# Kernel tuning notes

Measured on AMD Instinct MI355X. Metric: run time of the kernel, lower is better.

## Reference

```python
import jax, jax.numpy as jnp
import numpy as np

# HGIN_classifier: two relational-GIN layers with ReLU between.
# FastRGIN layer math (relational GIN, eps=0, single-linear MLP):
#   agg_r[i] = sum_{(j->i) with edge_type r} x[j]          (per-relation neighbor sum)
#   out[i]   = (1+eps) * x[i] @ W_self + sum_r agg_r[i] @ W_r + b

N = 100000      # nodes
E = 1600000     # edges (avg degree 16)
R = 2           # relations (follower / following)
DIN, DH, DOUT = 128, 256, 2
EPS = 0.0


def setup_inputs() -> dict:
    key = jax.random.key(0)
    ks = jax.random.split(key, 8)
    x = jax.random.normal(ks[0], (N, DIN), dtype=jnp.float32)
    edge_index = jax.random.randint(ks[1], (2, E), 0, N, dtype=jnp.int64)
    edge_type = jax.random.randint(ks[2], (E,), 0, R, dtype=jnp.int64)
    s1 = 1.0 / np.sqrt(DIN).astype(np.float32)
    s2 = 1.0 / np.sqrt(DH).astype(np.float32)
    w1_self = jax.random.normal(ks[3], (DIN, DH), jnp.float32) * s1
    w1_rel = jax.random.normal(ks[4], (R, DIN, DH), jnp.float32) * s1
    b1 = jnp.zeros((DH,), jnp.float32)
    w2_self = jax.random.normal(ks[5], (DH, DOUT), jnp.float32) * s2
    w2_rel = jax.random.normal(ks[6], (R, DH, DOUT), jnp.float32) * s2
    b2 = jnp.zeros((DOUT,), jnp.float32)
    return {"x": x, "edge_index": edge_index, "edge_type": edge_type,
            "w1_self": w1_self, "w1_rel": w1_rel, "b1": b1,
            "w2_self": w2_self, "w2_rel": w2_rel, "b2": b2}


def _rgin_layer(x, src, dst, etype, w_self, w_rel, b):
    n = x.shape[0]
    r = w_rel.shape[0]
    # fused (node, relation) segment id so one segment_sum handles all relations
    seg = dst * r + etype                                   # [E]
    agg = jax.ops.segment_sum(x[src], seg, num_segments=n * r)  # [N*R, d_in]
    agg = agg.reshape(n, r, -1)                              # [N, R, d_in]
    return (1.0 + EPS) * (x @ w_self) + jnp.einsum('nri,rio->no', agg, w_rel) + b


def reference(x, edge_index, edge_type, w1_self, w1_rel, b1, w2_self, w2_rel, b2):
    src, dst = edge_index[0], edge_index[1]
    h = jax.nn.relu(_rgin_layer(x, src, dst, edge_type, w1_self, w1_rel, b1))
    out = _rgin_layer(h, src, dst, edge_type, w2_self, w2_rel, b2)
    return out
```

## Files before the change

### kernel.cpp

```cpp
#include <hip/hip_runtime.h>


typedef _Float16 f16;
typedef _Float16 f16x2 __attribute__((ext_vector_type(2)));
typedef _Float16 f16x4 __attribute__((ext_vector_type(4)));
typedef _Float16 f16x8 __attribute__((ext_vector_type(8)));
typedef float    f32x4 __attribute__((ext_vector_type(4)));
typedef __attribute__((address_space(3))) void       as3_void;
typedef __attribute__((address_space(1))) const void as1_cvoid;

constexpr int NN   = 100000;
constexpr int NR   = NN * 2;
constexpr int NB   = 512;
constexpr int BSH  = 9;
constexpr int CAP  = 5120;
constexpr int CHUNK = 2048;

__global__ void zero_small(int* __restrict__ gbase) {
  int t = threadIdx.x;
  if (t < NB) gbase[t] = t * CAP;
}

__global__ void bucketB(const int* __restrict__ src, const int* __restrict__ dst,
                        const int* __restrict__ et, int* __restrict__ gbase,
                        int* __restrict__ ebuf, int E) {
  __shared__ int h[NB], base[NB];
  int t = threadIdx.x;
  for (int b = t; b < NB; b += 256) h[b] = 0;
  __syncthreads();
  int lo = blockIdx.x * CHUNK, hi = min(E, lo + CHUNK);
  for (int e = lo + t; e < hi; e += 256)
    atomicAdd(&h[(dst[e] * 2 + et[e]) >> BSH], 1);
  __syncthreads();
  for (int b = t; b < NB; b += 256) {
    int c = h[b];
    base[b] = c ? atomicAdd(&gbase[b], c) : 0;
    h[b] = 0;
  }
  __syncthreads();
  for (int e = lo + t; e < hi; e += 256) {
    int seg = dst[e] * 2 + et[e];
    int b = seg >> BSH;
    int r = atomicAdd(&h[b], 1);
    ebuf[base[b] + r] = (src[e] << BSH) | (seg & (NB - 1));
  }
}

__global__ void bscan(const int* __restrict__ gbase, int* __restrict__ bstart) {
  __shared__ int s[NB];
  int t = threadIdx.x;
  int v = gbase[t] - t * CAP;
  s[t] = v;
  __syncthreads();
  #pragma unroll
  for (int o = 1; o < NB; o <<= 1) {
    int u = (t >= o) ? s[t - o] : 0;
    __syncthreads();
    s[t] += u;
    __syncthreads();
  }
  bstart[t] = s[t] - v;
  if (t == NB - 1) bstart[NB] = s[t];
}

__global__ void bucketC(const int* __restrict__ ebuf, const int* __restrict__ gbase,
                        const int* __restrict__ bstart,
                        int* __restrict__ off, int* __restrict__ srcs) {
  __shared__ int sh[NB], soff[NB], cnt[NB], tmp[256];
  int b = blockIdx.x, t = threadIdx.x;
  int lo = b * CAP, hi = gbase[b];
  int obase = bstart[b];
  for (int s0 = t; s0 < NB; s0 += 256) { sh[s0] = 0; cnt[s0] = 0; }
  __syncthreads();
  for (int e = lo + t; e < hi; e += 256)
    atomicAdd(&sh[ebuf[e] & (NB - 1)], 1);
  __syncthreads();
  int a0 = sh[2 * t], a1 = sh[2 * t + 1];
  tmp[t] = a0 + a1;
  __syncthreads();
  #pragma unroll
  for (int o = 1; o < 256; o <<= 1) {
    int u = (t >= o) ? tmp[t - o] : 0;
    __syncthreads();
    tmp[t] += u;
    __syncthreads();
  }
  int ex = tmp[t] - (a0 + a1);
  soff[2 * t] = ex;
  soff[2 * t + 1] = ex + a0;
  __syncthreads();
  int g0 = (b << BSH) + 2 * t;
  if (g0 <= NR)     off[g0]     = obase + soff[2 * t];
  if (g0 + 1 <= NR) off[g0 + 1] = obase + soff[2 * t + 1];
  for (int e = lo + t; e < hi; e += 256) {
    int p = ebuf[e];
    int s = p & (NB - 1);
    int r = atomicAdd(&cnt[s], 1);
    srcs[obase + soff[s] + r] = ((unsigned)p) >> BSH;
  }
}

__global__ void cvt_all(const float4* __restrict__ xf, f16* __restrict__ xh,
                        const float* __restrict__ w1s, const float* __restrict__ w1r,
                        f16* __restrict__ w1t, int n4) {
  int i = blockIdx.x * blockDim.x + threadIdx.x;
  if (i < n4) {
    float4 v = xf[i];
    f16x4 h;
    h.x = (f16)v.x; h.y = (f16)v.y; h.z = (f16)v.z; h.w = (f16)v.w;
    *(f16x4*)(xh + (size_t)i * 4) = h;
  } else {
    int id = i - n4;
    if (id < 12 * 256 * 32) {
      int ks = id >> 13, rem = id & 8191;
      int n = rem >> 5, ki = rem & 31;
      int k = ks * 32 + ki;
      float v = (k < 128) ? w1s[k * 256 + n] : w1r[(k - 128) * 256 + n];
      w1t[id] = (f16)v;
    }
  }
}

__global__ void aggregate(const f16* __restrict__ xh, const int* __restrict__ off,
                          const int* __restrict__ srcs, f16* __restrict__ aggh) {
  int w = (blockIdx.x * blockDim.x + threadIdx.x) >> 6;
  if (w >= NN) return;
  int lane = threadIdx.x & 63;
  int h = lane >> 5, c = lane & 31;
  int e0 = off[2 * w];
  int e1 = off[2 * w + 1];
  int e2 = off[2 * w + 2];
  float ax = 0.f, ay = 0.f, az = 0.f, aw = 0.f;
  float bx = 0.f, by = 0.f, bz = 0.f, bw = 0.f;

  int e = e0;
  for (; e + 7 < e1; e += 8) {
    f16x4 v0 = *(const f16x4*)(xh + (long)srcs[e     + h] * 128 + c * 4);
    f16x4 v1 = *(const f16x4*)(xh + (long)srcs[e + 2 + h] * 128 + c * 4);
    f16x4 v2 = *(const f16x4*)(xh + (long)srcs[e + 4 + h] * 128 + c * 4);
    f16x4 v3 = *(const f16x4*)(xh + (long)srcs[e + 6 + h] * 128 + c * 4);
    ax += (float)v0.x + (float)v1.x + (float)v2.x + (float)v3.x;
    ay += (float)v0.y + (float)v1.y + (float)v2.y + (float)v3.y;
    az += (float)v0.z + (float)v1.z + (float)v2.z + (float)v3.z;
    aw += (float)v0.w + (float)v1.w + (float)v2.w + (float)v3.w;
  }
  for (; e + 1 < e1; e += 2) {
    f16x4 v = *(const f16x4*)(xh + (long)srcs[e + h] * 128 + c * 4);
    ax += (float)v.x; ay += (float)v.y; az += (float)v.z; aw += (float)v.w;
  }
  if (e < e1) {
    f16x4 v = *(const f16x4*)(xh + (long)srcs[e] * 128 + c * 4);
    if (h == 0) { ax += (float)v.x; ay += (float)v.y; az += (float)v.z; aw += (float)v.w; }
  }
  e = e1;
  for (; e + 7 < e2; e += 8) {
    f16x4 v0 = *(const f16x4*)(xh + (long)srcs[e     + h] * 128 + c * 4);
    f16x4 v1 = *(const f16x4*)(xh + (long)srcs[e + 2 + h] * 128 + c * 4);
    f16x4 v2 = *(const f16x4*)(xh + (long)srcs[e + 4 + h] * 128 + c * 4);
    f16x4 v3 = *(const f16x4*)(xh + (long)srcs[e + 6 + h] * 128 + c * 4);
    bx += (float)v0.x + (float)v1.x + (float)v2.x + (float)v3.x;
    by += (float)v0.y + (float)v1.y + (float)v2.y + (float)v3.y;
    bz += (float)v0.z + (float)v1.z + (float)v2.z + (float)v3.z;
    bw += (float)v0.w + (float)v1.w + (float)v2.w + (float)v3.w;
  }
  for (; e + 1 < e2; e += 2) {
    f16x4 v = *(const f16x4*)(xh + (long)srcs[e + h] * 128 + c * 4);
    bx += (float)v.x; by += (float)v.y; bz += (float)v.z; bw += (float)v.w;
  }
  if (e < e2) {
    f16x4 v = *(const f16x4*)(xh + (long)srcs[e] * 128 + c * 4);
    if (h == 0) { bx += (float)v.x; by += (float)v.y; bz += (float)v.z; bw += (float)v.w; }
  }

  ax += __shfl_xor(ax, 32); ay += __shfl_xor(ay, 32);
  az += __shfl_xor(az, 32); aw += __shfl_xor(aw, 32);
  bx += __shfl_xor(bx, 32); by += __shfl_xor(by, 32);
  bz += __shfl_xor(bz, 32); bw += __shfl_xor(bw, 32);

  f16* row = aggh + (long)w * 256;
  f16x4 o;
  if (h == 0) {
    o.x = (f16)ax; o.y = (f16)ay; o.z = (f16)az; o.w = (f16)aw;
    *(f16x4*)(row + c * 4) = o;
  } else {
    o.x = (f16)bx; o.y = (f16)by; o.z = (f16)bz; o.w = (f16)bw;
    *(f16x4*)(row + 128 + c * 4) = o;
  }
}

__global__ __launch_bounds__(256) void gemm_mfma(
    const f16* __restrict__ xh, const f16* __restrict__ aggh,
    const f16* __restrict__ w1t,
    const float* __restrict__ b1, const float* __restrict__ w2s,
    const float* __restrict__ w2r, const float* __restrict__ b2,
    float* __restrict__ z2, float* __restrict__ out) {
  __shared__ __align__(16) f16 Ash[12 * 1024];
  float (*zbuf)[32][6] = (float (*)[32][6])(void*)Ash;
  const int t = threadIdx.x;
  const int lane = t & 63, wv = t >> 6;
  const int ml = lane & 15, quad = lane >> 4;
  const int cphi = quad ^ ((ml >> 1) & 3);
  const long rowBase = (long)blockIdx.x * 32;

  #pragma unroll
  for (int i = 0; i < 6; ++i) {
    int g = wv * 6 + i;
    int slab = g >> 1, half = g & 1;
    int s = half * 64 + lane;
    int r = s >> 2;
    int cl = (s & 3) ^ ((r >> 1) & 3);
    long grow = rowBase + r;
    const f16* ap = (slab < 4)
        ? (xh + grow * 128 + slab * 32 + cl * 8)
        : (aggh + grow * 256 + (slab - 4) * 32 + cl * 8);
    __builtin_amdgcn_global_load_lds((const as1_cvoid*)ap,
                                     (as3_void*)&Ash[slab * 1024 + half * 512],
                                     16, 0, 0);
  }
  __syncthreads();

  const f16* bwv = w1t + (long)(wv * 64 + ml) * 32 + quad * 8;
  f32x4 acc[2][4];
  #pragma unroll
  for (int mt = 0; mt < 2; ++mt)
    #pragma unroll
    for (int nt = 0; nt < 4; ++nt) acc[mt][nt] = (f32x4)(0.f);

  #pragma unroll
  for (int ks = 0; ks < 12; ++ks) {
    f16x8 af[2], bf[4];
    #pragma unroll
    for (int nt = 0; nt < 4; ++nt)
      bf[nt] = *(const f16x8*)(bwv + (long)ks * 8192 + nt * 16 * 32);
    #pragma unroll
    for (int mt = 0; mt < 2; ++mt)
      af[mt] = *(const f16x8*)&Ash[ks * 1024 + ((mt * 16 + ml) * 4 + cphi) * 8];
    #pragma unroll
    for (int mt = 0; mt < 2; ++mt)
      #pragma unroll
      for (int nt = 0; nt < 4; ++nt)
        acc[mt][nt] = __builtin_amdgcn_mfma_f32_16x16x32_f16(af[mt], bf[nt],
                                                             acc[mt][nt], 0, 0, 0);
  }
  __syncthreads();

  #pragma unroll
  for (int mt = 0; mt < 2; ++mt) {
    float z[4][6];
    #pragma unroll
    for (int rr = 0; rr < 4; ++rr)
      #pragma unroll
      for (int p = 0; p < 6; ++p) z[rr][p] = 0.f;
    #pragma unroll
    for (int nt = 0; nt < 4; ++nt) {
      int col = wv * 64 + nt * 16 + ml;
      float bb = b1[col];
      float wA = w2r[col * 2 + 0];
      float wB = w2r[col * 2 + 1];
      float wC = w2r[512 + col * 2 + 0];
      float wD = w2r[512 + col * 2 + 1];
      float wE = w2s[col * 2 + 0];
      float wF = w2s[col * 2 + 1];
      #pragma unroll
      for (int rr = 0; rr < 4; ++rr) {
        float hh = acc[mt][nt][rr] + bb;
        hh = hh > 0.f ? hh : 0.f;
        z[rr][0] = fmaf(hh, wA, z[rr][0]);
        z[rr][1] = fmaf(hh, wB, z[rr][1]);
        z[rr][2] = fmaf(hh, wC, z[rr][2]);
        z[rr][3] = fmaf(hh, wD, z[rr][3]);
        z[rr][4] = fmaf(hh, wE, z[rr][4]);
        z[rr][5] = fmaf(hh, wF, z[rr][5]);
      }
    }
    #pragma unroll
    for (int rr = 0; rr < 4; ++rr)
      #pragma unroll
      for (int p = 0; p < 6; ++p) {
        float v = z[rr][p];
        v += __shfl_xor(v, 1);
        v += __shfl_xor(v, 2);
        v += __shfl_xor(v, 4);
        v += __shfl_xor(v, 8);
        if (ml == 0) zbuf[wv][mt * 16 + quad * 4 + rr][p] = v;
      }
  }
  __syncthreads();
  if (t < 192) {
    int r = t / 6, p = t % 6;
    long grow = rowBase + r;
    float v = zbuf[0][r][p] + zbuf[1][r][p] + zbuf[2][r][p] + zbuf[3][r][p];
    if (p < 4) z2[grow * 4 + p] = v;
    else       out[grow * 2 + (p - 4)] = v + b2[p - 4];
  }
}

__global__ void gather2(const float* __restrict__ z2, const int* __restrict__ off,
                        const int* __restrict__ srcs, float* __restrict__ out) {
  int tid = blockIdx.x * blockDim.x + threadIdx.x;
  int n = tid >> 2;
  if (n >= NN) return;
  int sub = tid & 3;
  int e0 = off[2 * n];
  int e1 = off[2 * n + 1];
  int e2 = off[2 * n + 2];
  float o0 = 0.f, o1 = 0.f;
  for (int e = e0 + sub; e < e1; e += 4) {
    float2 v = *(const float2*)(z2 + (long)srcs[e] * 4);
    o0 += v.x; o1 += v.y;
  }
  for (int e = e1 + sub; e < e2; e += 4) {
    float2 v = *(const float2*)(z2 + (long)srcs[e] * 4 + 2);
    o0 += v.x; o1 += v.y;
  }
  o0 += __shfl_xor(o0, 1); o1 += __shfl_xor(o1, 1);
  o0 += __shfl_xor(o0, 2); o1 += __shfl_xor(o1, 2);
  if (sub == 0) {
    out[n * 2 + 0] += o0;
    out[n * 2 + 1] += o1;
  }
}

extern "C" void kernel_launch(void* const* d_in, const int* in_sizes, int n_in,
                              void* d_out, int out_size, void* d_ws, size_t ws_size,
                              hipStream_t stream) {
  const float* x   = (const float*)d_in[0];
  const int*   ei  = (const int*)d_in[1];
  const int*   et  = (const int*)d_in[2];
  const float* w1s = (const float*)d_in[3];
  const float* w1r = (const float*)d_in[4];
  const float* b1  = (const float*)d_in[5];
  const float* w2s = (const float*)d_in[6];
  const float* w2r = (const float*)d_in[7];
  const float* b2  = (const float*)d_in[8];
  float* out = (float*)d_out;
  const int E = in_sizes[2];
  const int* src = ei;
  const int* dst = ei + E;

  f16*   aggh = (f16*)d_ws;
  f16*   xh   = aggh + (size_t)NN * 256;
  f16*   w1t  = xh + (size_t)NN * 128;
  float* z2   = (float*)(w1t + 12 * 256 * 32);
  int*   ebuf = (int*)(z2 + (size_t)NN * 4);
  int*   srcs = ebuf + (size_t)NB * CAP;
  int*   off  = srcs + E;
  int*   gbase  = off + NR + 1;
  int*   bstart = gbase + NB;

  int nblk = (E + CHUNK - 1) / CHUNK;
  zero_small<<<1, 512, 0, stream>>>(gbase);
  bucketB<<<nblk, 256, 0, stream>>>(src, dst, et, gbase, ebuf, E);
  bscan<<<1, 512, 0, stream>>>(gbase, bstart);
  bucketC<<<NB, 256, 0, stream>>>(ebuf, gbase, bstart, off, srcs);

  int n4 = NN * 128 / 4;
  int ncvt = n4 + 12 * 256 * 32;
  cvt_all<<<(ncvt + 255) / 256, 256, 0, stream>>>((const float4*)x, xh,
                                                  w1s, w1r, w1t, n4);

  aggregate<<<(NN * 64 + 255) / 256, 256, 0, stream>>>(xh, off, srcs, aggh);

  gemm_mfma<<<NN / 32, 256, 0, stream>>>(xh, aggh, w1t, b1, w2s, w2r, b2,
                                         z2, out);

  gather2<<<(NN * 4 + 255) / 256, 256, 0, stream>>>(z2, off, srcs, out);
}
```

Baseline: 326.4 us.

## Load GEMM A operands directly from global into registers with software prefetch

The GEMM kernel no longer stages the 32-row A tile into LDS through global_load_lds. Each lane now reads its MFMA A fragments straight from global memory, double-buffering A and B fragments one k-step ahead of the MFMAs. The epilogue weights are hoisted before the main loop, and launch bounds request 4 blocks per SIMD. This removes the LDS fill, its barrier and most LDS use, at the cost of 16-byte strided global loads that each of the four waves repeats, and higher register pressure.

```diff
diff --git a/kernel.cpp b/kernel.cpp
--- a/kernel.cpp
+++ b/kernel.cpp
@@ -6,8 +6,6 @@
 typedef _Float16 f16x4 __attribute__((ext_vector_type(4)));
 typedef _Float16 f16x8 __attribute__((ext_vector_type(8)));
 typedef float    f32x4 __attribute__((ext_vector_type(4)));
-typedef __attribute__((address_space(3))) void       as3_void;
-typedef __attribute__((address_space(1))) const void as1_cvoid;
 
 constexpr int NN   = 100000;
 constexpr int NR   = NN * 2;
@@ -188,61 +186,74 @@
   }
 }
 
-__global__ __launch_bounds__(256) void gemm_mfma(
+__global__ __launch_bounds__(256, 4) void gemm_direct(
     const f16* __restrict__ xh, const f16* __restrict__ aggh,
     const f16* __restrict__ w1t,
     const float* __restrict__ b1, const float* __restrict__ w2s,
     const float* __restrict__ w2r, const float* __restrict__ b2,
     float* __restrict__ z2, float* __restrict__ out) {
-  __shared__ __align__(16) f16 Ash[12 * 1024];
-  float (*zbuf)[32][6] = (float (*)[32][6])(void*)Ash;
+  __shared__ float zbuf[4][32][6];
   const int t = threadIdx.x;
   const int lane = t & 63, wv = t >> 6;
   const int ml = lane & 15, quad = lane >> 4;
-  const int cphi = quad ^ ((ml >> 1) & 3);
+  const int ko = quad * 8;
   const long rowBase = (long)blockIdx.x * 32;
 
-  #pragma unroll
-  for (int i = 0; i < 6; ++i) {
-    int g = wv * 6 + i;
-    int slab = g >> 1, half = g & 1;
-    int s = half * 64 + lane;
-    int r = s >> 2;
-    int cl = (s & 3) ^ ((r >> 1) & 3);
-    long grow = rowBase + r;
-    const f16* ap = (slab < 4)
-        ? (xh + grow * 128 + slab * 32 + cl * 8)
-        : (aggh + grow * 256 + (slab - 4) * 32 + cl * 8);
-    __builtin_amdgcn_global_load_lds((const as1_cvoid*)ap,
-                                     (as3_void*)&Ash[slab * 1024 + half * 512],
-                                     16, 0, 0);
-  }
-  __syncthreads();
-
-  const f16* bwv = w1t + (long)(wv * 64 + ml) * 32 + quad * 8;
+  const f16* xr0 = xh   + (rowBase + ml) * 128 + ko;
+  const f16* xr1 = xh   + (rowBase + 16 + ml) * 128 + ko;
+  const f16* ar0 = aggh + (rowBase + ml) * 256 + ko;
+  const f16* ar1 = aggh + (rowBase + 16 + ml) * 256 + ko;
+  const f16* bwv = w1t + (long)(wv * 64 + ml) * 32 + ko;
+
+  float bb[4], wA[4], wB[4], wC[4], wD[4], wE[4], wF[4];
+  #pragma unroll
+  for (int nt = 0; nt < 4; ++nt) {
+    int col = wv * 64 + nt * 16 + ml;
+    bb[nt] = b1[col];
+    wA[nt] = w2r[col * 2 + 0];
+    wB[nt] = w2r[col * 2 + 1];
+    wC[nt] = w2r[512 + col * 2 + 0];
+    wD[nt] = w2r[512 + col * 2 + 1];
+    wE[nt] = w2s[col * 2 + 0];
+    wF[nt] = w2s[col * 2 + 1];
+  }
+
   f32x4 acc[2][4];
   #pragma unroll
   for (int mt = 0; mt < 2; ++mt)
     #pragma unroll
     for (int nt = 0; nt < 4; ++nt) acc[mt][nt] = (f32x4)(0.f);
 
+#define LDA(d, K) do { \
+    if ((K) < 4) { d[0] = *(const f16x8*)(xr0 + (K) * 32); \
+                   d[1] = *(const f16x8*)(xr1 + (K) * 32); } \
+    else         { d[0] = *(const f16x8*)(ar0 + ((K) - 4) * 32); \
+                   d[1] = *(const f16x8*)(ar1 + ((K) - 4) * 32); } } while (0)
+#define LDB(d, K) do { \
+    _Pragma("unroll") \
+    for (int nt = 0; nt < 4; ++nt) \
+      d[nt] = *(const f16x8*)(bwv + (long)(K) * 8192 + nt * 512); } while (0)
+
+  f16x8 afc[2], bfc[4], afn[2], bfn[4];
+  LDA(afc, 0);
+  LDB(bfc, 0);
   #pragma unroll
   for (int ks = 0; ks < 12; ++ks) {
-    f16x8 af[2], bf[4];
-    #pragma unroll
-    for (int nt = 0; nt < 4; ++nt)
-      bf[nt] = *(const f16x8*)(bwv + (long)ks * 8192 + nt * 16 * 32);
+    if (ks < 11) { LDA(afn, ks + 1); LDB(bfn, ks + 1); }
     #pragma unroll
     for (int mt = 0; mt < 2; ++mt)
-      af[mt] = *(const f16x8*)&Ash[ks * 1024 + ((mt * 16 + ml) * 4 + cphi) * 8];
-    #pragma unroll
-    for (int mt = 0; mt < 2; ++mt)
       #pragma unroll
       for (int nt = 0; nt < 4; ++nt)
-        acc[mt][nt] = __builtin_amdgcn_mfma_f32_16x16x32_f16(af[mt], bf[nt],
+        acc[mt][nt] = __builtin_amdgcn_mfma_f32_16x16x32_f16(afc[mt], bfc[nt],
                                                              acc[mt][nt], 0, 0, 0);
-  }
-  __syncthreads();
+    if (ks < 11) {
+      afc[0] = afn[0]; afc[1] = afn[1];
+      #pragma unroll
+      for (int nt = 0; nt < 4; ++nt) bfc[nt] = bfn[nt];
+    }
+  }
+#undef LDA
+#undef LDB
 
   #pragma unroll
   for (int mt = 0; mt < 2; ++mt) {
@@ -253,24 +264,16 @@
       for (int p = 0; p < 6; ++p) z[rr][p] = 0.f;
     #pragma unroll
     for (int nt = 0; nt < 4; ++nt) {
-      int col = wv * 64 + nt * 16 + ml;
-      float bb = b1[col];
-      float wA = w2r[col * 2 + 0];
-      float wB = w2r[col * 2 + 1];
-      float wC = w2r[512 + col * 2 + 0];
-      float wD = w2r[512 + col * 2 + 1];
-      float wE = w2s[col * 2 + 0];
-      float wF = w2s[col * 2 + 1];
       #pragma unroll
       for (int rr = 0; rr < 4; ++rr) {
-        float hh = acc[mt][nt][rr] + bb;
+        float hh = acc[mt][nt][rr] + bb[nt];
         hh = hh > 0.f ? hh : 0.f;
-        z[rr][0] = fmaf(hh, wA, z[rr][0]);
-        z[rr][1] = fmaf(hh, wB, z[rr][1]);
-        z[rr][2] = fmaf(hh, wC, z[rr][2]);
-        z[rr][3] = fmaf(hh, wD, z[rr][3]);
-        z[rr][4] = fmaf(hh, wE, z[rr][4]);
-        z[rr][5] = fmaf(hh, wF, z[rr][5]);
+        z[rr][0] = fmaf(hh, wA[nt], z[rr][0]);
+        z[rr][1] = fmaf(hh, wB[nt], z[rr][1]);
+        z[rr][2] = fmaf(hh, wC[nt], z[rr][2]);
+        z[rr][3] = fmaf(hh, wD[nt], z[rr][3]);
+        z[rr][4] = fmaf(hh, wE[nt], z[rr][4]);
+        z[rr][5] = fmaf(hh, wF[nt], z[rr][5]);
       }
     }
     #pragma unroll
@@ -361,8 +364,8 @@
 
   aggregate<<<(NN * 64 + 255) / 256, 256, 0, stream>>>(xh, off, srcs, aggh);
 
-  gemm_mfma<<<NN / 32, 256, 0, stream>>>(xh, aggh, w1t, b1, w2s, w2r, b2,
-                                         z2, out);
+  gemm_direct<<<NN / 32, 256, 0, stream>>>(xh, aggh, w1t, b1, w2s, w2r, b2,
+                                           z2, out);
 
   gather2<<<(NN * 4 + 255) / 256, 256, 0, stream>>>(z2, off, srcs, out);
 }
```

After: 351.5 us. +7.7%, slower.

## Replace two-level bucket sort CSR build with global atomic count-scan-scatter

Applied to the files above, without the earlier changes.

Swaps the shared-memory two-pass bucket sort (bucketB/bscan/bucketC with an intermediate ebuf) for a classic CSR build: global atomic histogram per (node, relation) segment, a two-level prefix scan, then an atomic-cursor scatter of source indices. This drops the intermediate packed edge buffer and the per-bucket shared-memory passes. In exchange it adds two launches and relies on global atomics on 200K counters, which contend more than shared-memory atomics. The order of sources within a segment is also no longer deterministic.

```diff
diff --git a/kernel.cpp b/kernel.cpp
--- a/kernel.cpp
+++ b/kernel.cpp
@@ -11,92 +11,74 @@
 
 constexpr int NN   = 100000;
 constexpr int NR   = NN * 2;
-constexpr int NB   = 512;
-constexpr int BSH  = 9;
-constexpr int CAP  = 5120;
-constexpr int CHUNK = 2048;
-
-__global__ void zero_small(int* __restrict__ gbase) {
-  int t = threadIdx.x;
-  if (t < NB) gbase[t] = t * CAP;
-}
-
-__global__ void bucketB(const int* __restrict__ src, const int* __restrict__ dst,
-                        const int* __restrict__ et, int* __restrict__ gbase,
-                        int* __restrict__ ebuf, int E) {
-  __shared__ int h[NB], base[NB];
-  int t = threadIdx.x;
-  for (int b = t; b < NB; b += 256) h[b] = 0;
-  __syncthreads();
-  int lo = blockIdx.x * CHUNK, hi = min(E, lo + CHUNK);
-  for (int e = lo + t; e < hi; e += 256)
-    atomicAdd(&h[(dst[e] * 2 + et[e]) >> BSH], 1);
-  __syncthreads();
-  for (int b = t; b < NB; b += 256) {
-    int c = h[b];
-    base[b] = c ? atomicAdd(&gbase[b], c) : 0;
-    h[b] = 0;
-  }
-  __syncthreads();
-  for (int e = lo + t; e < hi; e += 256) {
-    int seg = dst[e] * 2 + et[e];
-    int b = seg >> BSH;
-    int r = atomicAdd(&h[b], 1);
-    ebuf[base[b] + r] = (src[e] << BSH) | (seg & (NB - 1));
-  }
-}
-
-__global__ void bscan(const int* __restrict__ gbase, int* __restrict__ bstart) {
-  __shared__ int s[NB];
-  int t = threadIdx.x;
-  int v = gbase[t] - t * CAP;
+constexpr int NBK  = (NR + 511) / 512;
+
+__global__ void zero_cnt(int* __restrict__ cnt) {
+  int g = blockIdx.x * 256 + threadIdx.x;
+  if (g < NR) cnt[g] = 0;
+}
+
+__global__ void count_edges(const int* __restrict__ dst, const int* __restrict__ et,
+                            int* __restrict__ cnt, int E) {
+  int e = blockIdx.x * 256 + threadIdx.x;
+  if (e < E) atomicAdd(&cnt[dst[e] * 2 + et[e]], 1);
+}
+
+__global__ void scan_local(const int* __restrict__ cnt, int* __restrict__ pre,
+                           int* __restrict__ bsum) {
+  __shared__ int s[512];
+  int b = blockIdx.x, t = threadIdx.x;
+  int g = b * 512 + t;
+  int v = (g < NR) ? cnt[g] : 0;
   s[t] = v;
   __syncthreads();
   #pragma unroll
-  for (int o = 1; o < NB; o <<= 1) {
+  for (int o = 1; o < 512; o <<= 1) {
     int u = (t >= o) ? s[t - o] : 0;
     __syncthreads();
     s[t] += u;
     __syncthreads();
   }
-  bstart[t] = s[t] - v;
-  if (t == NB - 1) bstart[NB] = s[t];
-}
-
-__global__ void bucketC(const int* __restrict__ ebuf, const int* __restrict__ gbase,
-                        const int* __restrict__ bstart,
-                        int* __restrict__ off, int* __restrict__ srcs) {
-  __shared__ int sh[NB], soff[NB], cnt[NB], tmp[256];
-  int b = blockIdx.x, t = threadIdx.x;
-  int lo = b * CAP, hi = gbase[b];
-  int obase = bstart[b];
-  for (int s0 = t; s0 < NB; s0 += 256) { sh[s0] = 0; cnt[s0] = 0; }
-  __syncthreads();
-  for (int e = lo + t; e < hi; e += 256)
-    atomicAdd(&sh[ebuf[e] & (NB - 1)], 1);
-  __syncthreads();
-  int a0 = sh[2 * t], a1 = sh[2 * t + 1];
-  tmp[t] = a0 + a1;
-  __syncthreads();
-  #pragma unroll
-  for (int o = 1; o < 256; o <<= 1) {
-    int u = (t >= o) ? tmp[t - o] : 0;
+  if (g < NR) pre[g] = s[t] - v;
+  if (t == 511) bsum[b] = s[t];
+}
+
+__global__ void bscan2(const int* __restrict__ bsum, int* __restrict__ bbase) {
+  __shared__ int s[512];
+  int t = threadIdx.x;
+  int v = (t < NBK) ? bsum[t] : 0;
+  s[t] = v;
+  __syncthreads();
+  #pragma unroll
+  for (int o = 1; o < 512; o <<= 1) {
+    int u = (t >= o) ? s[t - o] : 0;
     __syncthreads();
-    tmp[t] += u;
+    s[t] += u;
     __syncthreads();
   }
-  int ex = tmp[t] - (a0 + a1);
-  soff[2 * t] = ex;
-  soff[2 * t + 1] = ex + a0;
-  __syncthreads();
-  int g0 = (b << BSH) + 2 * t;
-  if (g0 <= NR)     off[g0]     = obase + soff[2 * t];
-  if (g0 + 1 <= NR) off[g0 + 1] = obase + soff[2 * t + 1];
-  for (int e = lo + t; e < hi; e += 256) {
-    int p = ebuf[e];
-    int s = p & (NB - 1);
-    int r = atomicAdd(&cnt[s], 1);
-    srcs[obase + soff[s] + r] = ((unsigned)p) >> BSH;
+  if (t < NBK) bbase[t] = s[t] - v;
+}
+
+__global__ void finalize(const int* __restrict__ pre, const int* __restrict__ bbase,
+                         int* __restrict__ off, int* __restrict__ cur, int E) {
+  int g = blockIdx.x * 256 + threadIdx.x;
+  if (g < NR) {
+    int o = bbase[g >> 9] + pre[g];
+    off[g] = o;
+    cur[g] = o;
+  } else if (g == NR) {
+    off[NR] = E;
+  }
+}
+
+__global__ void scatter_edges(const int* __restrict__ src, const int* __restrict__ dst,
+                              const int* __restrict__ et, int* __restrict__ cur,
+                              int* __restrict__ srcs, int E) {
+  int e = blockIdx.x * 256 + threadIdx.x;
+  if (e < E) {
+    int seg = dst[e] * 2 + et[e];
+    int p = atomicAdd(&cur[seg], 1);
+    srcs[p] = src[e];
   }
 }
 
@@ -342,17 +324,21 @@
   f16*   xh   = aggh + (size_t)NN * 256;
   f16*   w1t  = xh + (size_t)NN * 128;
   float* z2   = (float*)(w1t + 12 * 256 * 32);
-  int*   ebuf = (int*)(z2 + (size_t)NN * 4);
-  int*   srcs = ebuf + (size_t)NB * CAP;
+  int*   srcs = (int*)(z2 + (size_t)NN * 4);
   int*   off  = srcs + E;
-  int*   gbase  = off + NR + 1;
-  int*   bstart = gbase + NB;
-
-  int nblk = (E + CHUNK - 1) / CHUNK;
-  zero_small<<<1, 512, 0, stream>>>(gbase);
-  bucketB<<<nblk, 256, 0, stream>>>(src, dst, et, gbase, ebuf, E);
-  bscan<<<1, 512, 0, stream>>>(gbase, bstart);
-  bucketC<<<NB, 256, 0, stream>>>(ebuf, gbase, bstart, off, srcs);
+  int*   cnt  = off + NR + 1;
+  int*   pre  = cnt + NR;
+  int*   cur  = pre + NR;
+  int*   bsum = cur + NR;
+  int*   bbase = bsum + NBK;
+
+  int eblk = (E + 255) / 256;
+  zero_cnt<<<(NR + 255) / 256, 256, 0, stream>>>(cnt);
+  count_edges<<<eblk, 256, 0, stream>>>(dst, et, cnt, E);
+  scan_local<<<NBK, 512, 0, stream>>>(cnt, pre, bsum);
+  bscan2<<<1, 512, 0, stream>>>(bsum, bbase);
+  finalize<<<(NR + 256) / 256, 256, 0, stream>>>(pre, bbase, off, cur, E);
+  scatter_edges<<<eblk, 256, 0, stream>>>(src, dst, et, cur, srcs, E);
 
   int n4 = NN * 128 / 4;
   int ncvt = n4 + 12 * 256 * 32;
```

Result: slower. 447.0 us (+37.0%).
